# Kernel optimization log

Measured on AMD Instinct MI355X. Metric: run time of the kernel, lower is better.

The kernel has to match this reference:

```python
import jax, jax.numpy as jnp
import numpy as np

B, S, H = 8, 4096, 2048
TOP_K = 32


def setup_inputs() -> dict:
    key = jax.random.key(0)
    k1, k2, k3 = jax.random.split(key, 3)
    base = jax.random.normal(k1, (B, S, H), dtype=jnp.float32)
    batch_weights = jax.random.normal(k2, (B, 1, H), dtype=jnp.float32)
    intervention_positions = jax.random.randint(k3, (B, S), 0, S, dtype=jnp.int32)
    return {"base": base, "intervention_positions": intervention_positions,
            "batch_weights": batch_weights}


def reference(base, intervention_positions, batch_weights):
    # base: [B,S,H]; intervention_positions: [B,S]; batch_weights: [B,1,H]
    b, s, h = base.shape
    bidx = jnp.arange(b)[:, None]                                   # [B,1]
    # gather intervened hidden states: base[b, pos]  -> [B,S,H]
    gathered = jnp.take_along_axis(base, intervention_positions[..., None], axis=1)
    # psi(h) = ReLU(W h): rank-1 bmm with batch_weights -> [B,S]
    detect_latent = jax.nn.relu(
        jnp.einsum('bsh,bh->bs', gathered, batch_weights[:, 0, :]))
    topk_vals, topk_idx = jax.lax.top_k(detect_latent, TOP_K)       # [B,K]
    # zero out the top-k entries (scatter along last dim)
    non_topk_latents = detect_latent.at[bidx, topk_idx].set(0.0)
    # steering vector: mean(topk) * W  -> [B,1,H]
    steer = jnp.mean(topk_vals, axis=-1)[:, None, None] * batch_weights
    # scatter-add steering vector back at the intervened positions
    mixed_output = base.at[bidx, intervention_positions].add(
        jnp.broadcast_to(steer, (b, s, h)))
    return mixed_output, detect_latent, non_topk_latents
```

## Files before the change

### kernel.cpp

```cpp
#include <hip/hip_runtime.h>

#define TOPK 32

__global__ void detect_kernel(const float* __restrict__ base,
                              const int* __restrict__ pos,
                              const float* __restrict__ bw,
                              float* __restrict__ detect,
                              int* __restrict__ counts,
                              int S, int H) {
    int wid  = (blockIdx.x * blockDim.x + threadIdx.x) >> 6;
    int lane = threadIdx.x & 63;
    int b = wid / S;
    int s = wid - b * S;
    int p = pos[b * S + s];

    const float4* row = (const float4*)(base + ((size_t)b * S + p) * H);
    const float4* w4  = (const float4*)(bw + (size_t)b * H);
    int n4 = H >> 2;

    float acc = 0.f;
    for (int i = lane; i < n4; i += 64) {
        float4 v = row[i];
        float4 w = w4[i];
        acc += v.x * w.x + v.y * w.y + v.z * w.z + v.w * w.w;
    }
    for (int off = 32; off > 0; off >>= 1)
        acc += __shfl_down(acc, off, 64);

    if (lane == 0) {
        detect[b * S + s] = fmaxf(acc, 0.f);
        atomicAdd(&counts[b * S + p], 1);
    }
}

__global__ void topk_kernel(const float* __restrict__ detect,
                            float* __restrict__ nontopk,
                            float* __restrict__ meanv,
                            int S) {
    extern __shared__ float vals[];
    __shared__ float wval[4];
    __shared__ int   widx[4];

    int b = blockIdx.x;
    int t = threadIdx.x;

    for (int i = t; i < S; i += 256) vals[i] = detect[(size_t)b * S + i];
    __syncthreads();

    float sum = 0.f;
    for (int it = 0; it < TOPK; ++it) {
        float lv = -INFINITY;
        int   li = 0x7fffffff;
        for (int i = t; i < S; i += 256) {
            float v = vals[i];
            if (v > lv) { lv = v; li = i; }
        }
        for (int off = 32; off > 0; off >>= 1) {
            float ov = __shfl_down(lv, off, 64);
            int   oi = __shfl_down(li, off, 64);
            if (ov > lv || (ov == lv && oi < li)) { lv = ov; li = oi; }
        }
        int lane = t & 63, w = t >> 6;
        if (lane == 0) { wval[w] = lv; widx[w] = li; }
        __syncthreads();
        if (t == 0) {
            float bv = wval[0]; int bi = widx[0];
            for (int k = 1; k < 4; ++k)
                if (wval[k] > bv || (wval[k] == bv && widx[k] < bi)) { bv = wval[k]; bi = widx[k]; }
            sum += bv;
            vals[bi] = -INFINITY;
            if (it == TOPK - 1) meanv[b] = sum / (float)TOPK;
        }
        __syncthreads();
    }

    for (int i = t; i < S; i += 256) {
        float v = vals[i];
        nontopk[(size_t)b * S + i] = (v == -INFINITY) ? 0.f : v;
    }
}

__global__ void mix_kernel(const float* __restrict__ base,
                           const float* __restrict__ bw,
                           const int* __restrict__ counts,
                           const float* __restrict__ meanv,
                           float* __restrict__ mixed,
                           int S, int H) {
    int row = blockIdx.x;
    int b = row / S;
    float scale = (float)counts[row] * meanv[b];

    const float4* b4 = (const float4*)(base + (size_t)row * H);
    const float4* w4 = (const float4*)(bw + (size_t)b * H);
    float4*       o4 = (float4*)(mixed + (size_t)row * H);
    int n4 = H >> 2;

    for (int i = threadIdx.x; i < n4; i += blockDim.x) {
        float4 v = b4[i];
        float4 w = w4[i];
        v.x += scale * w.x;
        v.y += scale * w.y;
        v.z += scale * w.z;
        v.w += scale * w.w;
        o4[i] = v;
    }
}

extern "C" void kernel_launch(void* const* d_in, const int* in_sizes, int n_in,
                              void* d_out, int out_size, void* d_ws, size_t ws_size,
                              hipStream_t stream) {
    const float* base = (const float*)d_in[0];
    const int*   pos  = (const int*)d_in[1];
    const float* bw   = (const float*)d_in[2];

    long n0 = in_sizes[0];
    long n1 = in_sizes[1];
    long n2 = in_sizes[2];
    int H = (int)(n0 / n1);
    int B = (int)(n2 / H);
    int S = (int)(n1 / B);

    float* out_mixed   = (float*)d_out;
    float* out_detect  = out_mixed + (size_t)B * S * H;
    float* out_nontopk = out_detect + (size_t)B * S;

    int*   counts = (int*)d_ws;
    float* meanv  = (float*)((char*)d_ws + (size_t)B * S * sizeof(int));

    hipMemsetAsync(counts, 0, (size_t)B * S * sizeof(int), stream);

    int nwaves = B * S;
    detect_kernel<<<nwaves / 4, 256, 0, stream>>>(base, pos, bw, out_detect, counts, S, H);
    topk_kernel<<<B, 256, (size_t)S * sizeof(float), stream>>>(out_detect, out_nontopk, meanv, S);
    mix_kernel<<<B * S, 256, 0, stream>>>(base, bw, counts, meanv, out_mixed, S, H);
}
```

Baseline: 189.0 us.

## Move position counting into top-k, single-wave top-k, multi-row nontemporal mix

Computes the per-position scatter counts with shared-memory atomics inside the top-k kernel, which removes the memset and the global atomics in the detect kernel. The top-k selection now runs on a single wave with float4 LDS scans and shuffle broadcasts, so the per-iteration block barriers are gone. The mix kernel handles four rows per block and writes the output with nontemporal stores, and the loops get unroll pragmas. The cost is that three of the four waves sit idle during top-k and the top-k launch needs twice the shared memory.

```diff
diff --git a/kernel.cpp b/kernel.cpp
--- a/kernel.cpp
+++ b/kernel.cpp
@@ -1,82 +1,92 @@
 #include <hip/hip_runtime.h>
 
 #define TOPK 32
+
+typedef float vfloat4 __attribute__((ext_vector_type(4)));
 
 __global__ void detect_kernel(const float* __restrict__ base,
                               const int* __restrict__ pos,
                               const float* __restrict__ bw,
                               float* __restrict__ detect,
-                              int* __restrict__ counts,
                               int S, int H) {
     int wid  = (blockIdx.x * blockDim.x + threadIdx.x) >> 6;
     int lane = threadIdx.x & 63;
     int b = wid / S;
-    int s = wid - b * S;
-    int p = pos[b * S + s];
+    int p = pos[wid];
 
     const float4* row = (const float4*)(base + ((size_t)b * S + p) * H);
     const float4* w4  = (const float4*)(bw + (size_t)b * H);
     int n4 = H >> 2;
 
     float acc = 0.f;
+    #pragma unroll 8
     for (int i = lane; i < n4; i += 64) {
         float4 v = row[i];
         float4 w = w4[i];
         acc += v.x * w.x + v.y * w.y + v.z * w.z + v.w * w.w;
     }
+    #pragma unroll
     for (int off = 32; off > 0; off >>= 1)
         acc += __shfl_down(acc, off, 64);
 
-    if (lane == 0) {
-        detect[b * S + s] = fmaxf(acc, 0.f);
-        atomicAdd(&counts[b * S + p], 1);
-    }
+    if (lane == 0) detect[wid] = fmaxf(acc, 0.f);
 }
 
 __global__ void topk_kernel(const float* __restrict__ detect,
+                            const int* __restrict__ pos,
                             float* __restrict__ nontopk,
+                            int* __restrict__ counts,
                             float* __restrict__ meanv,
                             int S) {
-    extern __shared__ float vals[];
-    __shared__ float wval[4];
-    __shared__ int   widx[4];
+    extern __shared__ float smem[];
+    float* vals = smem;
+    int*   cnt  = (int*)(smem + S);
 
     int b = blockIdx.x;
     int t = threadIdx.x;
+    int T = blockDim.x;
 
-    for (int i = t; i < S; i += 256) vals[i] = detect[(size_t)b * S + i];
+    for (int i = t; i < S; i += T) {
+        vals[i] = detect[(size_t)b * S + i];
+        cnt[i] = 0;
+    }
+    __syncthreads();
+    for (int i = t; i < S; i += T)
+        atomicAdd(&cnt[pos[(size_t)b * S + i]], 1);
     __syncthreads();
 
-    float sum = 0.f;
-    for (int it = 0; it < TOPK; ++it) {
-        float lv = -INFINITY;
-        int   li = 0x7fffffff;
-        for (int i = t; i < S; i += 256) {
-            float v = vals[i];
-            if (v > lv) { lv = v; li = i; }
+    if (t < 64) {
+        int lane = t;
+        float sum = 0.f;
+        for (int it = 0; it < TOPK; ++it) {
+            float lv = -INFINITY;
+            int   li = 0x7fffffff;
+            for (int c = lane * 4; c < S; c += 256) {
+                float4 v = *(const float4*)&vals[c];
+                if (v.x > lv) { lv = v.x; li = c; }
+                if (v.y > lv) { lv = v.y; li = c + 1; }
+                if (v.z > lv) { lv = v.z; li = c + 2; }
+                if (v.w > lv) { lv = v.w; li = c + 3; }
+            }
+            #pragma unroll
+            for (int off = 32; off > 0; off >>= 1) {
+                float ov = __shfl_down(lv, off, 64);
+                int   oi = __shfl_down(li, off, 64);
+                if (ov > lv || (ov == lv && oi < li)) { lv = ov; li = oi; }
+            }
+            lv = __shfl(lv, 0, 64);
+            li = __shfl(li, 0, 64);
+            sum += lv;
+            if (lane == 0) vals[li] = -INFINITY;
         }
-        for (int off = 32; off > 0; off >>= 1) {
-            float ov = __shfl_down(lv, off, 64);
-            int   oi = __shfl_down(li, off, 64);
-            if (ov > lv || (ov == lv && oi < li)) { lv = ov; li = oi; }
-        }
-        int lane = t & 63, w = t >> 6;
-        if (lane == 0) { wval[w] = lv; widx[w] = li; }
-        __syncthreads();
-        if (t == 0) {
-            float bv = wval[0]; int bi = widx[0];
-            for (int k = 1; k < 4; ++k)
-                if (wval[k] > bv || (wval[k] == bv && widx[k] < bi)) { bv = wval[k]; bi = widx[k]; }
-            sum += bv;
-            vals[bi] = -INFINITY;
-            if (it == TOPK - 1) meanv[b] = sum / (float)TOPK;
-        }
-        __syncthreads();
+        if (lane == 0) meanv[b] = sum / (float)TOPK;
     }
+    __syncthreads();
 
-    for (int i = t; i < S; i += 256) {
+    for (int i = t; i < S; i += T) {
         float v = vals[i];
         nontopk[(size_t)b * S + i] = (v == -INFINITY) ? 0.f : v;
+        counts[(size_t)b * S + i] = cnt[i];
     }
 }
 
@@ -86,23 +96,27 @@
                            const float* __restrict__ meanv,
                            float* __restrict__ mixed,
                            int S, int H) {
-    int row = blockIdx.x;
-    int b = row / S;
-    float scale = (float)counts[row] * meanv[b];
-
-    const float4* b4 = (const float4*)(base + (size_t)row * H);
+    int r0 = blockIdx.x << 2;
+    int b  = r0 / S;
     const float4* w4 = (const float4*)(bw + (size_t)b * H);
-    float4*       o4 = (float4*)(mixed + (size_t)row * H);
+    float mb = meanv[b];
     int n4 = H >> 2;
 
-    for (int i = threadIdx.x; i < n4; i += blockDim.x) {
-        float4 v = b4[i];
-        float4 w = w4[i];
-        v.x += scale * w.x;
-        v.y += scale * w.y;
-        v.z += scale * w.z;
-        v.w += scale * w.w;
-        o4[i] = v;
+    for (int r = r0; r < r0 + 4; ++r) {
+        float scale = (float)counts[r] * mb;
+        const float4* b4 = (const float4*)(base + (size_t)r * H);
+        vfloat4*      o4 = (vfloat4*)(mixed + (size_t)r * H);
+        #pragma unroll 2
+        for (int i = threadIdx.x; i < n4; i += blockDim.x) {
+            float4 v = b4[i];
+            float4 w = w4[i];
+            vfloat4 o;
+            o.x = v.x + scale * w.x;
+            o.y = v.y + scale * w.y;
+            o.z = v.z + scale * w.z;
+            o.w = v.w + scale * w.w;
+            __builtin_nontemporal_store(o, &o4[i]);
+        }
     }
 }
 
@@ -127,10 +141,9 @@
     int*   counts = (int*)d_ws;
     float* meanv  = (float*)((char*)d_ws + (size_t)B * S * sizeof(int));
 
-    hipMemsetAsync(counts, 0, (size_t)B * S * sizeof(int), stream);
-
-    int nwaves = B * S;
-    detect_kernel<<<nwaves / 4, 256, 0, stream>>>(base, pos, bw, out_detect, counts, S, H);
-    topk_kernel<<<B, 256, (size_t)S * sizeof(float), stream>>>(out_detect, out_nontopk, meanv, S);
-    mix_kernel<<<B * S, 256, 0, stream>>>(base, bw, counts, meanv, out_mixed, S, H);
+    int nrows = B * S;
+    detect_kernel<<<nrows / 4, 256, 0, stream>>>(base, pos, bw, out_detect, S, H);
+    topk_kernel<<<B, 256, 2 * (size_t)S * sizeof(float), stream>>>(
+        out_detect, pos, out_nontopk, counts, meanv, S);
+    mix_kernel<<<nrows / 4, 256, 0, stream>>>(base, bw, counts, meanv, out_mixed, S, H);
 }
```

Measured after the change: 186.2 us. About the same (-1.5%).
